# Kernel optimization log

Hardware: AMD Instinct MI355X
Metric: run time of the kernel (lower is better)

## Reference

```python
import jax, jax.numpy as jnp
import numpy as np

N_NODES = 50000
N_EDGES = 800000
IN_DIM, HID_DIM, OUT_DIM = 128, 128, 64


def setup_inputs() -> dict:
    key = jax.random.key(0)
    ks = jax.random.split(key, 12)
    x = jax.random.normal(ks[0], (N_NODES, IN_DIM), dtype=jnp.float32)
    src = jax.random.randint(ks[1], (N_EDGES,), 0, N_NODES, dtype=jnp.int32)
    dst = jax.random.randint(ks[2], (N_EDGES,), 0, N_NODES, dtype=jnp.int32)
    def lin(k, fan_in, fan_out):
        s = 1.0 / np.sqrt(fan_in)
        kw, kb = jax.random.split(k)
        W = jax.random.uniform(kw, (fan_in, fan_out), jnp.float32, -s, s)
        b = jax.random.uniform(kb, (fan_out,), jnp.float32, -s, s)
        return W, b
    W1, b1 = lin(ks[3], IN_DIM, HID_DIM)
    W2, b2 = lin(ks[4], HID_DIM, HID_DIM)
    W3, b3 = lin(ks[5], HID_DIM, OUT_DIM)
    Wf, bf = lin(ks[6], OUT_DIM, 1)
    return {"x": x, "src": src, "dst": dst,
            "W1": W1, "b1": b1, "W2": W2, "b2": b2,
            "W3": W3, "b3": b3, "Wf": Wf, "bf": bf}


def reference(x, src, dst, W1, b1, W2, b2, W3, b3, Wf, bf):
    n = x.shape[0]
    # GCN symmetric norm with self-loops: deg = in-degree + 1 (self loop)
    ones = jnp.ones(src.shape[0], x.dtype)
    deg = jax.ops.segment_sum(ones, dst, num_segments=n) + 1.0
    dinv = jax.lax.rsqrt(deg)                       # [N]
    edge_norm = dinv[src] * dinv[dst]               # [E]
    self_norm = dinv * dinv                         # [N], self-loop weight

    def gcn(h, W, b):
        h = h @ W                                   # transform first (PyG order)
        agg = jax.ops.segment_sum(h[src] * edge_norm[:, None], dst, num_segments=n)
        agg = agg + h * self_norm[:, None]          # self-loop contribution
        return agg + b

    h = jax.nn.relu(gcn(x, W1, b1))
    h = jax.nn.relu(gcn(h, W2, b2))
    h = jax.nn.relu(gcn(h, W3, b3))
    return h @ Wf + bf                              # [N, 1] per-node scores
```

## Files before the change

kernel.cpp:

```cpp
#include <hip/hip_runtime.h>
#include <hip/hip_bf16.h>

typedef short bf16x8 __attribute__((ext_vector_type(8)));
typedef float f32x4 __attribute__((ext_vector_type(4)));
typedef _Float16 f16x2 __attribute__((ext_vector_type(2)));

static __device__ __forceinline__ unsigned short f2bf_rne(float f) {
    unsigned int u = __float_as_uint(f);
    u += 0x7fff + ((u >> 16) & 1);
    return (unsigned short)(u >> 16);
}
static __device__ __forceinline__ float bf2f(unsigned short h) {
    return __uint_as_float(((unsigned int)h) << 16);
}

static __device__ __forceinline__ void wsplit_one(const float* W, unsigned short* hi,
                                                  unsigned short* lo, int BN, int idx) {
    int k = idx / BN, n = idx % BN;
    float w = W[idx];
    unsigned short h = f2bf_rne(w);
    unsigned short l = f2bf_rne(w - bf2f(h));
    int CT = BN >> 4;
    int kc = k >> 5, quad = (k >> 3) & 3, j = k & 7;
    int ct = n >> 4, c = n & 15;
    int slot = (((kc * CT + ct) * 4 + quad) * 16 + c) * 8 + j;
    hi[slot] = h;
    lo[slot] = l;
}


template<int BN>
static __device__ __forceinline__ void gemm_body(const float* __restrict__ A,
                        const unsigned short* __restrict__ Whi, const unsigned short* __restrict__ Wlo,
                        _Float16* __restrict__ C, int N, int blk,
                        unsigned short* AhiS, unsigned short* AloS) {
    constexpr int CT = BN / 16;
    const int tid = threadIdx.x;
    const int wave = tid >> 6;
    const int lane = tid & 63;
    const int quad = lane >> 4;
    const int c16 = lane & 15;
    const int row0 = blk * 64;

    f32x4 acc[CT];
    #pragma unroll
    for (int t = 0; t < CT; ++t) acc[t] = (f32x4){0.f, 0.f, 0.f, 0.f};

    for (int kc = 0; kc < 4; ++kc) {
        #pragma unroll
        for (int r = 0; r < 2; ++r) {
            int f4 = tid + r * 256;
            int arow = f4 >> 3;
            int c4 = f4 & 7;
            int grow = row0 + arow;
            float4 v = make_float4(0.f, 0.f, 0.f, 0.f);
            if (grow < N) v = *(const float4*)&A[(size_t)grow * 128 + kc * 32 + c4 * 4];
            unsigned short h0 = f2bf_rne(v.x), h1 = f2bf_rne(v.y), h2 = f2bf_rne(v.z), h3 = f2bf_rne(v.w);
            ushort4 hv = make_ushort4(h0, h1, h2, h3);
            ushort4 lv = make_ushort4(f2bf_rne(v.x - bf2f(h0)), f2bf_rne(v.y - bf2f(h1)),
                                      f2bf_rne(v.z - bf2f(h2)), f2bf_rne(v.w - bf2f(h3)));
            int q = c4 >> 1;
            int joff = (c4 & 1) * 4;
            int base = (q * 64 + arow) * 8 + joff;
            *(ushort4*)&AhiS[base] = hv;
            *(ushort4*)&AloS[base] = lv;
        }
        __syncthreads();

        int abase = (quad * 64 + wave * 16 + c16) * 8;
        bf16x8 ahi = *(const bf16x8*)&AhiS[abase];
        bf16x8 alo = *(const bf16x8*)&AloS[abase];

        #pragma unroll
        for (int ct = 0; ct < CT; ++ct) {
            size_t bslot = ((size_t)(kc * CT + ct) * 64 + lane) * 8;
            bf16x8 bhi = *(const bf16x8*)&Whi[bslot];
            bf16x8 blo = *(const bf16x8*)&Wlo[bslot];
            acc[ct] = __builtin_amdgcn_mfma_f32_16x16x32_bf16(ahi, bhi, acc[ct], 0, 0, 0);
            acc[ct] = __builtin_amdgcn_mfma_f32_16x16x32_bf16(ahi, blo, acc[ct], 0, 0, 0);
            acc[ct] = __builtin_amdgcn_mfma_f32_16x16x32_bf16(alo, bhi, acc[ct], 0, 0, 0);
        }
        __syncthreads();
    }

    #pragma unroll
    for (int ct = 0; ct < CT; ++ct) {
        #pragma unroll
        for (int r = 0; r < 4; ++r) {
            int grow = row0 + wave * 16 + quad * 4 + r;
            if (grow < N) C[(size_t)grow * BN + ct * 16 + c16] = (_Float16)acc[ct][r];
        }
    }
}


__global__ __launch_bounds__(256) void k_count_wsplit(const int* __restrict__ dst, int* __restrict__ deg,
                          int* __restrict__ rank,
                          const float* __restrict__ W1, const float* __restrict__ W2, const float* __restrict__ W3,
                          unsigned short* __restrict__ W1hi, unsigned short* __restrict__ W1lo,
                          unsigned short* __restrict__ W2hi, unsigned short* __restrict__ W2lo,
                          unsigned short* __restrict__ W3hi, unsigned short* __restrict__ W3lo,
                          int E) {
    int e = blockIdx.x * blockDim.x + threadIdx.x;
    if (e < E) rank[e] = atomicAdd(&deg[dst[e]], 1);
    if (e < 128 * 128) {
        wsplit_one(W1, W1hi, W1lo, 128, e);
        wsplit_one(W2, W2hi, W2lo, 128, e);
    }
    if (e < 128 * 64) wsplit_one(W3, W3hi, W3lo, 64, e);
}

__global__ __launch_bounds__(1024) void k_scan(const int* __restrict__ deg, float* __restrict__ dinv,
                                               int* __restrict__ row_start, int N) {
    __shared__ int s[1024];
    __shared__ int wsum[16];
    __shared__ int prefix;
    const int t = threadIdx.x;
    const int base = blockIdx.x * 1024;

    {
        int v = 0;
        for (int j = t; j < base; j += 1024) v += deg[j];
        for (int off = 32; off > 0; off >>= 1) v += __shfl_down(v, off, 64);
        if ((t & 63) == 0) wsum[t >> 6] = v;
        __syncthreads();
        if (t == 0) {
            int acc = 0;
            #pragma unroll
            for (int k = 0; k < 16; ++k) acc += wsum[k];
            prefix = acc;
        }
    }

    int i = base + t;
    int v = 0;
    if (i < N) {
        v = deg[i];
        dinv[i] = rsqrtf((float)v + 1.0f);
    }
    s[t] = v;
    __syncthreads();
    for (int off = 1; off < 1024; off <<= 1) {
        int x = (t >= off) ? s[t - off] : 0;
        __syncthreads();
        s[t] += x;
        __syncthreads();
    }
    if (i <= N) row_start[i] = prefix + s[t] - v;
}


__global__ __launch_bounds__(256, 2) void k_gemm1_scatter(const float* __restrict__ A,
                          const unsigned short* __restrict__ Whi, const unsigned short* __restrict__ Wlo,
                          _Float16* __restrict__ C, int N, int gemmGrid,
                          const int* __restrict__ src, const int* __restrict__ dst,
                          const int* __restrict__ row_start, const int* __restrict__ rank,
                          const float* __restrict__ dinv, int2* __restrict__ cv, int E) {
    __shared__ unsigned short AhiS[4 * 64 * 8];
    __shared__ unsigned short AloS[4 * 64 * 8];
    if ((int)blockIdx.x < gemmGrid) {
        gemm_body<128>(A, Whi, Wlo, C, N, blockIdx.x, AhiS, AloS);
    } else {
        int e = (blockIdx.x - gemmGrid) * 256 + threadIdx.x;
        if (e < E) {
            int d = dst[e];
            int s = src[e];
            cv[row_start[d] + rank[e]] = make_int2(s, __float_as_int(dinv[s]));
        }
    }
}

template<int BN>
__global__ __launch_bounds__(256, 2) void k_gemm_mfma(const float* __restrict__ A,
                        const unsigned short* __restrict__ Whi, const unsigned short* __restrict__ Wlo,
                        _Float16* __restrict__ C, int N) {
    __shared__ unsigned short AhiS[4 * 64 * 8];
    __shared__ unsigned short AloS[4 * 64 * 8];
    gemm_body<BN>(A, Whi, Wlo, C, N, blockIdx.x, AhiS, AloS);
}


__global__ __launch_bounds__(256) void k_agg128(const _Float16* __restrict__ t, float* __restrict__ outp,
                      const int* __restrict__ row_start, const int2* __restrict__ cv,
                      const float* __restrict__ dinv, const float* __restrict__ bias,
                      int N) {
    int gid = blockIdx.x * blockDim.x + threadIdx.x;
    int node = gid >> 6;
    int lane = gid & 63;
    if (node >= N) return;
    int p = row_start[node];
    int end = row_start[node + 1];
    const f16x2* tp = (const f16x2*)t;
    float2 acc[4];
    #pragma unroll
    for (int j = 0; j < 4; ++j) acc[j] = make_float2(0.f, 0.f);

    while (p < end) {
        int idx = p + lane;
        int2 h = (idx < end) ? cv[idx] : make_int2(0, 0);
        int cnt = min(end - p, 64);
        int rounds = (cnt + 15) >> 4;
        for (int r = 0; r < rounds; ++r) {
            int base = r * 16;
            int s[16]; float w[16];
            #pragma unroll
            for (int j = 0; j < 16; ++j) {
                s[j] = __builtin_amdgcn_readlane(h.x, base + j);
                w[j] = __int_as_float(__builtin_amdgcn_readlane(h.y, base + j));
            }
            f16x2 v[16];
            #pragma unroll
            for (int j = 0; j < 16; ++j) v[j] = tp[s[j] * 64 + lane];
            #pragma unroll
            for (int j = 0; j < 16; ++j) {
                acc[j & 3].x += w[j] * (float)v[j].x;
                acc[j & 3].y += w[j] * (float)v[j].y;
            }
        }
        p += 64;
    }
    float di = dinv[node];
    f16x2 sv = tp[node * 64 + lane];
    float2 bv = ((const float2*)bias)[lane];
    float sx = (acc[0].x + acc[1].x) + (acc[2].x + acc[3].x);
    float sy = (acc[0].y + acc[1].y) + (acc[2].y + acc[3].y);
    float2 r;
    r.x = fmaxf(di * sx + di * di * (float)sv.x + bv.x, 0.f);
    r.y = fmaxf(di * sy + di * di * (float)sv.y + bv.y, 0.f);
    ((float2*)outp)[node * 64 + lane] = r;
}

__global__ __launch_bounds__(256) void k_agg64_final(const _Float16* __restrict__ t, float* __restrict__ outp,
                      const int* __restrict__ row_start, const int2* __restrict__ cv,
                      const float* __restrict__ dinv, const float* __restrict__ bias,
                      const float* __restrict__ Wf, const float* __restrict__ bf,
                      int N) {
    int gid = blockIdx.x * blockDim.x + threadIdx.x;
    int node = gid >> 6;
    int lane = gid & 63;
    if (node >= N) return;
    int p = row_start[node];
    int end = row_start[node + 1];
    float acc[4] = {0.f, 0.f, 0.f, 0.f};

    while (p < end) {
        int idx = p + lane;
        int2 h = (idx < end) ? cv[idx] : make_int2(0, 0);
        int cnt = min(end - p, 64);
        int rounds = (cnt + 15) >> 4;
        for (int r = 0; r < rounds; ++r) {
            int base = r * 16;
            int s[16]; float w[16];
            #pragma unroll
            for (int j = 0; j < 16; ++j) {
                s[j] = __builtin_amdgcn_readlane(h.x, base + j);
                w[j] = __int_as_float(__builtin_amdgcn_readlane(h.y, base + j));
            }
            _Float16 v[16];
            #pragma unroll
            for (int j = 0; j < 16; ++j) v[j] = t[s[j] * 64 + lane];
            #pragma unroll
            for (int j = 0; j < 16; ++j) acc[j & 3] += w[j] * (float)v[j];
        }
        p += 64;
    }
    float di = dinv[node];
    float r = di * ((acc[0] + acc[1]) + (acc[2] + acc[3])) + di * di * (float)t[node * 64 + lane] + bias[lane];
    r = fmaxf(r, 0.f);
    float v = r * Wf[lane];
    for (int off = 32; off > 0; off >>= 1) v += __shfl_down(v, off, 64);
    if (lane == 0) outp[node] = v + bf[0];
}


extern "C" void kernel_launch(void* const* d_in, const int* in_sizes, int n_in,
                              void* d_out, int out_size, void* d_ws, size_t ws_size,
                              hipStream_t stream) {
    const float* x  = (const float*)d_in[0];
    const int*   src = (const int*)d_in[1];
    const int*   dst = (const int*)d_in[2];
    const float* W1 = (const float*)d_in[3];
    const float* b1 = (const float*)d_in[4];
    const float* W2 = (const float*)d_in[5];
    const float* b2 = (const float*)d_in[6];
    const float* W3 = (const float*)d_in[7];
    const float* b3 = (const float*)d_in[8];
    const float* Wf = (const float*)d_in[9];
    const float* bf = (const float*)d_in[10];
    float* out = (float*)d_out;

    const int N = 50000;
    const int E = 800000;

    char* ws = (char*)d_ws;
    size_t off = 0;
    auto alloc = [&](size_t bytes) -> void* {
        void* p = (void*)(ws + off);
        off += (bytes + 511) & ~((size_t)511);
        return p;
    };
    int*   deg       = (int*)alloc((size_t)N * 4);
    float* dinv      = (float*)alloc((size_t)N * 4);
    int*   row_start = (int*)alloc((size_t)(N + 1) * 4);
    int*   rank      = (int*)alloc((size_t)E * 4);
    int2*  cv        = (int2*)alloc((size_t)E * 8);
    _Float16* bufT   = (_Float16*)alloc((size_t)N * 128 * 2);
    float* bufH      = (float*)alloc((size_t)N * 128 * 4);
    unsigned short* W1hi = (unsigned short*)alloc(128 * 128 * 2);
    unsigned short* W1lo = (unsigned short*)alloc(128 * 128 * 2);
    unsigned short* W2hi = (unsigned short*)alloc(128 * 128 * 2);
    unsigned short* W2lo = (unsigned short*)alloc(128 * 128 * 2);
    unsigned short* W3hi = (unsigned short*)alloc(128 * 64 * 2);
    unsigned short* W3lo = (unsigned short*)alloc(128 * 64 * 2);

    hipMemsetAsync(deg, 0, (size_t)N * 4, stream);

    k_count_wsplit<<<(E + 255) / 256, 256, 0, stream>>>(dst, deg, rank, W1, W2, W3,
                                                        W1hi, W1lo, W2hi, W2lo, W3hi, W3lo, E);
    int NB = (N + 1023) / 1024;
    k_scan<<<NB, 1024, 0, stream>>>(deg, dinv, row_start, N);

    int gemmGrid = (N + 63) / 64;
    int scatGrid = (E + 255) / 256;
    int aggGrid = (N * 64 + 255) / 256;

    k_gemm1_scatter<<<gemmGrid + scatGrid, 256, 0, stream>>>(x, W1hi, W1lo, bufT, N, gemmGrid,
                                                             src, dst, row_start, rank, dinv, cv, E);
    k_agg128<<<aggGrid, 256, 0, stream>>>(bufT, bufH, row_start, cv, dinv, b1, N);
    k_gemm_mfma<128><<<gemmGrid, 256, 0, stream>>>(bufH, W2hi, W2lo, bufT, N);
    k_agg128<<<aggGrid, 256, 0, stream>>>(bufT, bufH, row_start, cv, dinv, b2, N);
    k_gemm_mfma<64><<<gemmGrid, 256, 0, stream>>>(bufH, W3hi, W3lo, bufT, N);
    k_agg64_final<<<aggGrid, 256, 0, stream>>>(bufT, out, row_start, cv, dinv, b3, Wf, bf, N);
}
```

Before: 276.3 us.

## Pre-split GEMM inputs into packed bf16 hi/lo and drop LDS staging

GEMM inputs are stored as packed u32 words holding the hi and lo bf16 halves. The aggregation kernel writes them that way, and the count kernel converts x into this form. The GEMM loads its A fragments straight into registers and unpacks them with shifts, which removes the shared-memory staging, the barriers and the per-tile conversion work. In exchange it adds a full extra read/write pass over x, uses strided per-lane global loads, and raises the occupancy target in the launch bounds.

Result: no change. 278.1 us (+0.6%).

```diff
diff --git a/kernel.cpp b/kernel.cpp
--- a/kernel.cpp
+++ b/kernel.cpp
@@ -4,6 +4,7 @@
 typedef short bf16x8 __attribute__((ext_vector_type(8)));
 typedef float f32x4 __attribute__((ext_vector_type(4)));
 typedef _Float16 f16x2 __attribute__((ext_vector_type(2)));
+typedef unsigned int u32;
 
 static __device__ __forceinline__ unsigned short f2bf_rne(float f) {
     unsigned int u = __float_as_uint(f);
@@ -12,6 +13,11 @@
 }
 static __device__ __forceinline__ float bf2f(unsigned short h) {
     return __uint_as_float(((unsigned int)h) << 16);
+}
+static __device__ __forceinline__ u32 packsplit(float f) {
+    unsigned short h = f2bf_rne(f);
+    unsigned short l = f2bf_rne(f - bf2f(h));
+    return ((u32)h << 16) | l;
 }
 
 static __device__ __forceinline__ void wsplit_one(const float* W, unsigned short* hi,
@@ -30,10 +36,9 @@
 
 
 template<int BN>
-static __device__ __forceinline__ void gemm_body(const float* __restrict__ A,
+static __device__ __forceinline__ void gemm_body(const u32* __restrict__ A,
                         const unsigned short* __restrict__ Whi, const unsigned short* __restrict__ Wlo,
-                        _Float16* __restrict__ C, int N, int blk,
-                        unsigned short* AhiS, unsigned short* AloS) {
+                        _Float16* __restrict__ C, int N, int blk) {
     constexpr int CT = BN / 16;
     const int tid = threadIdx.x;
     const int wave = tid >> 6;
@@ -42,45 +47,43 @@
     const int c16 = lane & 15;
     const int row0 = blk * 64;
 
+    const int arow = row0 + wave * 16 + c16;
+    const bool valid = arow < N;
+    const u32* ar = A + (size_t)arow * 128;
+
+    uint4 a[8];
+    #pragma unroll
+    for (int i = 0; i < 8; ++i) {
+        int off = (i >> 1) * 32 + quad * 8 + (i & 1) * 4;
+        a[i] = valid ? *(const uint4*)&ar[off] : make_uint4(0, 0, 0, 0);
+    }
+
     f32x4 acc[CT];
     #pragma unroll
     for (int t = 0; t < CT; ++t) acc[t] = (f32x4){0.f, 0.f, 0.f, 0.f};
 
+    #pragma unroll
     for (int kc = 0; kc < 4; ++kc) {
-        #pragma unroll
-        for (int r = 0; r < 2; ++r) {
-            int f4 = tid + r * 256;
-            int arow = f4 >> 3;
-            int c4 = f4 & 7;
-            int grow = row0 + arow;
-            float4 v = make_float4(0.f, 0.f, 0.f, 0.f);
-            if (grow < N) v = *(const float4*)&A[(size_t)grow * 128 + kc * 32 + c4 * 4];
-            unsigned short h0 = f2bf_rne(v.x), h1 = f2bf_rne(v.y), h2 = f2bf_rne(v.z), h3 = f2bf_rne(v.w);
-            ushort4 hv = make_ushort4(h0, h1, h2, h3);
-            ushort4 lv = make_ushort4(f2bf_rne(v.x - bf2f(h0)), f2bf_rne(v.y - bf2f(h1)),
-                                      f2bf_rne(v.z - bf2f(h2)), f2bf_rne(v.w - bf2f(h3)));
-            int q = c4 >> 1;
-            int joff = (c4 & 1) * 4;
-            int base = (q * 64 + arow) * 8 + joff;
-            *(ushort4*)&AhiS[base] = hv;
-            *(ushort4*)&AloS[base] = lv;
-        }
-        __syncthreads();
-
-        int abase = (quad * 64 + wave * 16 + c16) * 8;
-        bf16x8 ahi = *(const bf16x8*)&AhiS[abase];
-        bf16x8 alo = *(const bf16x8*)&AloS[abase];
+        uint4 a0 = a[kc * 2], a1 = a[kc * 2 + 1];
+        union { u32 u[4]; bf16x8 v; } hi, lo;
+        hi.u[0] = (a0.x >> 16) | (a0.y & 0xffff0000u);
+        hi.u[1] = (a0.z >> 16) | (a0.w & 0xffff0000u);
+        hi.u[2] = (a1.x >> 16) | (a1.y & 0xffff0000u);
+        hi.u[3] = (a1.z >> 16) | (a1.w & 0xffff0000u);
+        lo.u[0] = (a0.x & 0xffffu) | (a0.y << 16);
+        lo.u[1] = (a0.z & 0xffffu) | (a0.w << 16);
+        lo.u[2] = (a1.x & 0xffffu) | (a1.y << 16);
+        lo.u[3] = (a1.z & 0xffffu) | (a1.w << 16);
 
         #pragma unroll
         for (int ct = 0; ct < CT; ++ct) {
             size_t bslot = ((size_t)(kc * CT + ct) * 64 + lane) * 8;
             bf16x8 bhi = *(const bf16x8*)&Whi[bslot];
             bf16x8 blo = *(const bf16x8*)&Wlo[bslot];
-            acc[ct] = __builtin_amdgcn_mfma_f32_16x16x32_bf16(ahi, bhi, acc[ct], 0, 0, 0);
-            acc[ct] = __builtin_amdgcn_mfma_f32_16x16x32_bf16(ahi, blo, acc[ct], 0, 0, 0);
-            acc[ct] = __builtin_amdgcn_mfma_f32_16x16x32_bf16(alo, bhi, acc[ct], 0, 0, 0);
-        }
-        __syncthreads();
+            acc[ct] = __builtin_amdgcn_mfma_f32_16x16x32_bf16(hi.v, bhi, acc[ct], 0, 0, 0);
+            acc[ct] = __builtin_amdgcn_mfma_f32_16x16x32_bf16(hi.v, blo, acc[ct], 0, 0, 0);
+            acc[ct] = __builtin_amdgcn_mfma_f32_16x16x32_bf16(lo.v, bhi, acc[ct], 0, 0, 0);
+        }
     }
 
     #pragma unroll
@@ -96,18 +99,30 @@
 
 __global__ __launch_bounds__(256) void k_count_wsplit(const int* __restrict__ dst, int* __restrict__ deg,
                           int* __restrict__ rank,
+                          const float* __restrict__ x, u32* __restrict__ xsplit,
                           const float* __restrict__ W1, const float* __restrict__ W2, const float* __restrict__ W3,
                           unsigned short* __restrict__ W1hi, unsigned short* __restrict__ W1lo,
                           unsigned short* __restrict__ W2hi, unsigned short* __restrict__ W2lo,
                           unsigned short* __restrict__ W3hi, unsigned short* __restrict__ W3lo,
-                          int E) {
+                          int E, int nElem) {
     int e = blockIdx.x * blockDim.x + threadIdx.x;
+    int gsz = gridDim.x * blockDim.x;
     if (e < E) rank[e] = atomicAdd(&deg[dst[e]], 1);
     if (e < 128 * 128) {
         wsplit_one(W1, W1hi, W1lo, 128, e);
         wsplit_one(W2, W2hi, W2lo, 128, e);
     }
     if (e < 128 * 64) wsplit_one(W3, W3hi, W3lo, 64, e);
+    int nF4 = nElem >> 2;
+    for (int i = e; i < nF4; i += gsz) {
+        float4 v = ((const float4*)x)[i];
+        uint4 p;
+        p.x = packsplit(v.x);
+        p.y = packsplit(v.y);
+        p.z = packsplit(v.z);
+        p.w = packsplit(v.w);
+        ((uint4*)xsplit)[i] = p;
+    }
 }
 
 __global__ __launch_bounds__(1024) void k_scan(const int* __restrict__ deg, float* __restrict__ dinv,
@@ -150,16 +165,14 @@
 }
 
 
-__global__ __launch_bounds__(256, 2) void k_gemm1_scatter(const float* __restrict__ A,
+__global__ __launch_bounds__(256, 3) void k_gemm1_scatter(const u32* __restrict__ A,
                           const unsigned short* __restrict__ Whi, const unsigned short* __restrict__ Wlo,
                           _Float16* __restrict__ C, int N, int gemmGrid,
                           const int* __restrict__ src, const int* __restrict__ dst,
                           const int* __restrict__ row_start, const int* __restrict__ rank,
                           const float* __restrict__ dinv, int2* __restrict__ cv, int E) {
-    __shared__ unsigned short AhiS[4 * 64 * 8];
-    __shared__ unsigned short AloS[4 * 64 * 8];
     if ((int)blockIdx.x < gemmGrid) {
-        gemm_body<128>(A, Whi, Wlo, C, N, blockIdx.x, AhiS, AloS);
+        gemm_body<128>(A, Whi, Wlo, C, N, blockIdx.x);
     } else {
         int e = (blockIdx.x - gemmGrid) * 256 + threadIdx.x;
         if (e < E) {
@@ -171,16 +184,14 @@
 }
 
 template<int BN>
-__global__ __launch_bounds__(256, 2) void k_gemm_mfma(const float* __restrict__ A,
+__global__ __launch_bounds__(256, 3) void k_gemm_mfma(const u32* __restrict__ A,
                         const unsigned short* __restrict__ Whi, const unsigned short* __restrict__ Wlo,
                         _Float16* __restrict__ C, int N) {
-    __shared__ unsigned short AhiS[4 * 64 * 8];
-    __shared__ unsigned short AloS[4 * 64 * 8];
-    gemm_body<BN>(A, Whi, Wlo, C, N, blockIdx.x, AhiS, AloS);
-}
-
-
-__global__ __launch_bounds__(256) void k_agg128(const _Float16* __restrict__ t, float* __restrict__ outp,
+    gemm_body<BN>(A, Whi, Wlo, C, N, blockIdx.x);
+}
+
+
+__global__ __launch_bounds__(256) void k_agg128(const _Float16* __restrict__ t, u32* __restrict__ outp,
                       const int* __restrict__ row_start, const int2* __restrict__ cv,
                       const float* __restrict__ dinv, const float* __restrict__ bias,
                       int N) {
@@ -224,10 +235,9 @@
     float2 bv = ((const float2*)bias)[lane];
     float sx = (acc[0].x + acc[1].x) + (acc[2].x + acc[3].x);
     float sy = (acc[0].y + acc[1].y) + (acc[2].y + acc[3].y);
-    float2 r;
-    r.x = fmaxf(di * sx + di * di * (float)sv.x + bv.x, 0.f);
-    r.y = fmaxf(di * sy + di * di * (float)sv.y + bv.y, 0.f);
-    ((float2*)outp)[node * 64 + lane] = r;
+    float rx = fmaxf(di * sx + di * di * (float)sv.x + bv.x, 0.f);
+    float ry = fmaxf(di * sy + di * di * (float)sv.y + bv.y, 0.f);
+    ((uint2*)outp)[node * 64 + lane] = make_uint2(packsplit(rx), packsplit(ry));
 }
 
 __global__ __launch_bounds__(256) void k_agg64_final(const _Float16* __restrict__ t, float* __restrict__ outp,
@@ -304,8 +314,9 @@
     int*   row_start = (int*)alloc((size_t)(N + 1) * 4);
     int*   rank      = (int*)alloc((size_t)E * 4);
     int2*  cv        = (int2*)alloc((size_t)E * 8);
+    u32*   xsplit    = (u32*)alloc((size_t)N * 128 * 4);
     _Float16* bufT   = (_Float16*)alloc((size_t)N * 128 * 2);
-    float* bufH      = (float*)alloc((size_t)N * 128 * 4);
+    u32*   bufH      = (u32*)alloc((size_t)N * 128 * 4);
     unsigned short* W1hi = (unsigned short*)alloc(128 * 128 * 2);
     unsigned short* W1lo = (unsigned short*)alloc(128 * 128 * 2);
     unsigned short* W2hi = (unsigned short*)alloc(128 * 128 * 2);
@@ -315,8 +326,9 @@
 
     hipMemsetAsync(deg, 0, (size_t)N * 4, stream);
 
-    k_count_wsplit<<<(E + 255) / 256, 256, 0, stream>>>(dst, deg, rank, W1, W2, W3,
-                                                        W1hi, W1lo, W2hi, W2lo, W3hi, W3lo, E);
+    k_count_wsplit<<<(E + 255) / 256, 256, 0, stream>>>(dst, deg, rank, x, xsplit, W1, W2, W3,
+                                                        W1hi, W1lo, W2hi, W2lo, W3hi, W3lo,
+                                                        E, N * 128);
     int NB = (N + 1023) / 1024;
     k_scan<<<NB, 1024, 0, stream>>>(deg, dinv, row_start, N);
 
@@ -324,7 +336,7 @@
     int scatGrid = (E + 255) / 256;
     int aggGrid = (N * 64 + 255) / 256;
 
-    k_gemm1_scatter<<<gemmGrid + scatGrid, 256, 0, stream>>>(x, W1hi, W1lo, bufT, N, gemmGrid,
+    k_gemm1_scatter<<<gemmGrid + scatGrid, 256, 0, stream>>>(xsplit, W1hi, W1lo, bufT, N, gemmGrid,
                                                              src, dst, row_start, rank, dinv, cv, E);
     k_agg128<<<aggGrid, 256, 0, stream>>>(bufT, bufH, row_start, cv, dinv, b1, N);
     k_gemm_mfma<128><<<gemmGrid, 256, 0, stream>>>(bufH, W2hi, W2lo, bufT, N);
```
